# Performance work log

Hardware: AMD Instinct MI355X
Metric: run time of the kernel (lower is better)

## Reference

```python
import jax, jax.numpy as jnp
import numpy as np

EMB = 768
HEADS = 8
HEAD_DIM = EMB // HEADS  # 96


def setup_inputs() -> dict:
    key = jax.random.key(0)
    k1, k2, k3, k4, k5 = jax.random.split(key, 5)
    N, S = 2, 4096
    values = jax.random.normal(k1, (N, S, EMB), dtype=jnp.float32)
    keys = jax.random.normal(k2, (N, S, EMB), dtype=jnp.float32)
    query = jax.random.normal(k3, (N, S, EMB), dtype=jnp.float32)
    # fc_out: nn.Linear(emb_size, emb_size) -> weight [out,in], bias [out]
    bound = 1.0 / np.sqrt(EMB)
    fc_w = jax.random.uniform(k4, (EMB, EMB), dtype=jnp.float32, minval=-bound, maxval=bound)
    fc_b = jax.random.uniform(k5, (EMB,), dtype=jnp.float32, minval=-bound, maxval=bound)
    return {"values": values, "keys": keys, "query": query, "fc_w": fc_w, "fc_b": fc_b}


def reference(values, keys, query, fc_w, fc_b):
    # NOTE: original forward never uses the per-head q/k/v Linear layers;
    # it reshapes raw inputs into heads directly. We reproduce that faithfully.
    N, Sq, _ = query.shape
    # [N, S, E] -> [N, H, S, D]
    q = query.reshape(N, Sq, HEADS, HEAD_DIM).transpose(0, 2, 1, 3)
    k = keys.reshape(N, -1, HEADS, HEAD_DIM).transpose(0, 2, 1, 3)
    v = values.reshape(N, -1, HEADS, HEAD_DIM).transpose(0, 2, 1, 3)
    scale = 1.0 / np.sqrt(HEAD_DIM).astype(np.float32)
    scores = jnp.einsum('nhqd,nhkd->nhqk', q, k) * scale  # [N,H,Sq,Sk]
    p = jax.nn.softmax(scores, axis=-1)
    x = jnp.einsum('nhqk,nhkd->nhqd', p, v)  # [N,H,Sq,D]
    x = x.transpose(0, 2, 1, 3).reshape(N, Sq, EMB)
    return x @ fc_w.T + fc_b
```

## Files before the change

kernel.cpp:

```cpp
#include <hip/hip_runtime.h>
#include <hip/hip_bf16.h>

#define S_LEN 4096
#define EMB 768
#define NHEAD 8
#define HDIM 96

typedef short bf16x8 __attribute__((ext_vector_type(8)));
typedef float f32x4 __attribute__((ext_vector_type(4)));
typedef float f32x16 __attribute__((ext_vector_type(16)));

__device__ __forceinline__ short f2bf(float x) {
  union { float f; unsigned u; } v; v.f = x;
  unsigned r = v.u + 0x7fffu + ((v.u >> 16) & 1u);
  return (short)(r >> 16);
}

__device__ __forceinline__ short f2bfh(float x) {
  union { __hip_bfloat16 h; short s; } u;
  u.h = __float2bfloat16(x);
  return u.s;
}

#define GLOAD_LDS16(gp, lp)                                              \
  __builtin_amdgcn_global_load_lds(                                      \
      (const __attribute__((address_space(1))) unsigned int*)(gp),       \
      (__attribute__((address_space(3))) unsigned int*)(lp), 16, 0, 0)

__global__ __launch_bounds__(256) void prep_kernel(const float* __restrict__ K,
                                                   const float* __restrict__ W,
                                                   const float* __restrict__ V,
                                                   short* __restrict__ KVT,
                                                   short* __restrict__ Wb) {
  __shared__ short tlbuf[6656];
  int b = blockIdx.x;
  int tid = threadIdx.x;
  if (b < 288) {
    int t = b * 256 + tid;
    size_t off = (size_t)t * 8;
    float4 a = *(const float4*)(W + off);
    float4 bq = *(const float4*)(W + off + 4);
    bf16x8 r;
    r[0]=f2bf(a.x);  r[1]=f2bf(a.y);  r[2]=f2bf(a.z);  r[3]=f2bf(a.w);
    r[4]=f2bf(bq.x); r[5]=f2bf(bq.y); r[6]=f2bf(bq.z); r[7]=f2bf(bq.w);
    *(bf16x8*)(Wb + off) = r;
    return;
  }
  int bb = b - 288;
  int n = bb >> 9, h = (bb >> 6) & 7, st = bb & 63;
  int s0 = st * 64;
  short* KVp = KVT + ((size_t)((n * NHEAD + h) * 64 + st)) * 12288;

  const float* kp = K + ((size_t)(n * S_LEN + s0)) * EMB + h * HDIM;
  #pragma unroll
  for (int k = 0; k < 6; ++k) {
    int idx = k * 256 + tid;
    int fidx = idx * 4;
    int s = fidx / 96, d = fidx % 96;
    float4 a = *(const float4*)(kp + (size_t)s * EMB + d);
    short* t4 = &tlbuf[s * 104 + d];
    t4[0] = f2bf(a.x); t4[1] = f2bf(a.y); t4[2] = f2bf(a.z); t4[3] = f2bf(a.w);
  }
  __syncthreads();
  #pragma unroll
  for (int i = 0; i < 3; ++i) {
    int u = i * 256 + tid;
    int c = u >> 7, rem = u & 127, key = rem >> 1, h8 = rem & 1;
    int db = c * 16 + h8 * 8;
    short4 lo = *(const short4*)&tlbuf[key * 104 + db];
    short4 hi4 = *(const short4*)&tlbuf[key * 104 + db + 4];
    bf16x8 r;
    r[0]=lo.x; r[1]=lo.y; r[2]=lo.z; r[3]=lo.w;
    r[4]=hi4.x; r[5]=hi4.y; r[6]=hi4.z; r[7]=hi4.w;
    *(bf16x8*)(KVp + (size_t)u * 8) = r;
  }
  __syncthreads();

  const float* vp = V + ((size_t)(n * S_LEN + s0)) * EMB + h * HDIM;
  #pragma unroll
  for (int k = 0; k < 6; ++k) {
    int idx = k * 256 + tid;
    int fidx = idx * 4;
    int s = fidx / 96, d = fidx % 96;
    float4 a = *(const float4*)(vp + (size_t)s * EMB + d);
    tlbuf[(d + 0) * 68 + s] = f2bf(a.x);
    tlbuf[(d + 1) * 68 + s] = f2bf(a.y);
    tlbuf[(d + 2) * 68 + s] = f2bf(a.z);
    tlbuf[(d + 3) * 68 + s] = f2bf(a.w);
  }
  __syncthreads();
  #pragma unroll
  for (int i = 0; i < 3; ++i) {
    int u = i * 256 + tid;
    int slice = u / 192;
    int rem = u - slice * 192;
    int dt = rem >> 6, hi2 = (rem >> 5) & 1, d5 = rem & 31;
    int d = dt * 32 + d5;
    int kb = 16 * slice + 4 * hi2;
    short4 lo = *(const short4*)&tlbuf[d * 68 + kb];
    short4 hi4 = *(const short4*)&tlbuf[d * 68 + kb + 8];
    bf16x8 r;
    r[0]=lo.x; r[1]=lo.y; r[2]=lo.z; r[3]=lo.w;
    r[4]=hi4.x; r[5]=hi4.y; r[6]=hi4.z; r[7]=hi4.w;
    *(bf16x8*)(KVp + 6144 + (size_t)u * 8) = r;
  }
}

template<int NKG>
__global__ __launch_bounds__(256, 3) void attn_kernel(const float* __restrict__ Q,
                                                      const short* __restrict__ KVT,
                                                      short* __restrict__ Xb,
                                                      float* __restrict__ Op,
                                                      float* __restrict__ lp) {
  __shared__ __align__(16) char smem[49152];
  constexpr int ITERS = S_LEN / NKG / 64;
  int L = blockIdx.x;
  int bb = L & 511;
  int kg = L >> 9;
  int h = bb & 7, j = bb >> 3;
  int n = j >> 5, qt = j & 31;
  int q0 = qt * 128;
  int tid = threadIdx.x;
  int w = tid >> 6, lane = tid & 63, l31 = lane & 31, hi = lane >> 5;

  const float kAdj = 0.14724512f;
  bf16x8 qf[6];
  {
    const float* qp = Q + ((size_t)(n * S_LEN + q0 + w * 32 + l31)) * EMB + h * HDIM + 8 * hi;
    #pragma unroll
    for (int c = 0; c < 6; ++c) {
      float4 a = *(const float4*)(qp + 16 * c);
      float4 bq = *(const float4*)(qp + 16 * c + 4);
      bf16x8 r;
      r[0]=f2bf(a.x*kAdj);  r[1]=f2bf(a.y*kAdj);  r[2]=f2bf(a.z*kAdj);  r[3]=f2bf(a.w*kAdj);
      r[4]=f2bf(bq.x*kAdj); r[5]=f2bf(bq.y*kAdj); r[6]=f2bf(bq.z*kAdj); r[7]=f2bf(bq.w*kAdj);
      qf[c] = r;
    }
  }

  const short* gKV = KVT + ((size_t)((n * NHEAD + h) * 64 + kg * ITERS)) * 12288
                        + (size_t)(w * 6) * 512 + lane * 8;
  char* ldsw = smem + w * 6144;

  #pragma unroll
  for (int i = 0; i < 6; ++i)
    GLOAD_LDS16(gKV + i * 512, ldsw + i * 1024);
  __syncthreads();

  f32x16 o[3];
  #pragma unroll
  for (int dt = 0; dt < 3; ++dt) o[dt] = (f32x16){};
  float tsl = 0.f;

  int cur = 0;
  #pragma unroll 1
  for (int t = 0; t < ITERS; ++t) {
    if (t < ITERS - 1) {
      const short* src = gKV + (size_t)(t + 1) * 12288;
      char* dst = ldsw + (cur ^ 1) * 24576;
      #pragma unroll
      for (int i = 0; i < 6; ++i)
        GLOAD_LDS16(src + i * 512, dst + i * 1024);
    }
    const char* kbl = smem + cur * 24576;
    const char* vbl = kbl + 12288;

    f32x16 s0 = (f32x16){}, s1 = (f32x16){};
    __builtin_amdgcn_s_setprio(1);
    #pragma unroll
    for (int c = 0; c < 6; ++c) {
      bf16x8 kf = *(const bf16x8*)(kbl + c * 2048 + l31 * 32 + hi * 16);
      s0 = __builtin_amdgcn_mfma_f32_32x32x16_bf16(kf, qf[c], s0, 0, 0, 0);
    }
    #pragma unroll
    for (int c = 0; c < 6; ++c) {
      bf16x8 kf = *(const bf16x8*)(kbl + c * 2048 + 1024 + l31 * 32 + hi * 16);
      s1 = __builtin_amdgcn_mfma_f32_32x32x16_bf16(kf, qf[c], s1, 0, 0, 0);
    }
    __builtin_amdgcn_s_setprio(0);

    #pragma unroll
    for (int r = 0; r < 16; ++r) { s0[r] = __builtin_amdgcn_exp2f(s0[r]); tsl += s0[r]; }
    #pragma unroll
    for (int r = 0; r < 16; ++r) { s1[r] = __builtin_amdgcn_exp2f(s1[r]); tsl += s1[r]; }

    #pragma unroll
    for (int ksub = 0; ksub < 2; ++ksub) {
      const f32x16& s = ksub ? s1 : s0;
      #pragma unroll
      for (int ks = 0; ks < 2; ++ks) {
        unsigned d0, d1, d2, d3;
        asm("v_cvt_pk_bf16_f32 %0, %1, %2" : "=v"(d0) : "v"(s[8*ks+0]), "v"(s[8*ks+1]));
        asm("v_cvt_pk_bf16_f32 %0, %1, %2" : "=v"(d1) : "v"(s[8*ks+2]), "v"(s[8*ks+3]));
        asm("v_cvt_pk_bf16_f32 %0, %1, %2" : "=v"(d2) : "v"(s[8*ks+4]), "v"(s[8*ks+5]));
        asm("v_cvt_pk_bf16_f32 %0, %1, %2" : "=v"(d3) : "v"(s[8*ks+6]), "v"(s[8*ks+7]));
        union { unsigned u[4]; bf16x8 v; } pu;
        pu.u[0] = d0; pu.u[1] = d1; pu.u[2] = d2; pu.u[3] = d3;
        int slice = 2 * ksub + ks;
        __builtin_amdgcn_s_setprio(1);
        #pragma unroll
        for (int dt = 0; dt < 3; ++dt) {
          bf16x8 vf = *(const bf16x8*)(vbl + (slice * 3 + dt) * 1024 + hi * 512 + l31 * 16);
          o[dt] = __builtin_amdgcn_mfma_f32_32x32x16_bf16(pu.v, vf, o[dt], 0, 0, 0);
        }
        __builtin_amdgcn_s_setprio(0);
      }
    }
    __syncthreads();
    cur ^= 1;
  }

  float lcol = tsl + __shfl_xor(tsl, 32, 64);

  if constexpr (NKG > 1) {
    float* op = Op + (size_t)L * 12288;
    #pragma unroll
    for (int p = 0; p < 4; ++p) {
      #pragma unroll
      for (int jj = 0; jj < 4; ++jj) {
        int qrow = w * 32 + 8 * p + 4 * hi + jj;
        op[(size_t)qrow * 96 + l31]      = o[0][4*p+jj];
        op[(size_t)qrow * 96 + 32 + l31] = o[1][4*p+jj];
        op[(size_t)qrow * 96 + 64 + l31] = o[2][4*p+jj];
      }
    }
    if (hi == 0) lp[(size_t)L * 128 + w * 32 + l31] = lcol;
  } else {
    __syncthreads();
    float* bcf = (float*)smem;
    if (hi == 0) bcf[w * 32 + l31] = 1.0f / lcol;
    __syncthreads();
    #pragma unroll
    for (int p = 0; p < 4; ++p) {
      #pragma unroll
      for (int jj = 0; jj < 4; ++jj) {
        int qr = 8 * p + 4 * hi + jj;
        float iv = bcf[w * 32 + qr];
        short* xp = Xb + ((size_t)(n * S_LEN + q0 + w * 32 + qr)) * EMB + h * HDIM + l31;
        xp[0]  = f2bfh(o[0][4*p+jj] * iv);
        xp[32] = f2bfh(o[1][4*p+jj] * iv);
        xp[64] = f2bfh(o[2][4*p+jj] * iv);
      }
    }
  }
}

__global__ __launch_bounds__(256) void combine_kernel(const float* __restrict__ Op,
                                                      const float* __restrict__ lp,
                                                      short* __restrict__ Xb,
                                                      int nkg) {
  int b = blockIdx.x;
  int h = b & 7, j = b >> 3, n = j >> 5, qt = j & 31;
  int q0 = qt * 128;
  int tid = threadIdx.x;
  #pragma unroll 1
  for (int i = 0; i < 12; ++i) {
    int idx = (i * 256 + tid) * 4;
    int qr = idx / 96, d = idx - qr * 96;
    float ax = 0.f, ay = 0.f, az = 0.f, aw = 0.f, l = 0.f;
    for (int kg = 0; kg < nkg; ++kg) {
      size_t blk = (size_t)(kg * 512 + b);
      float4 v = *(const float4*)(Op + blk * 12288 + idx);
      ax += v.x; ay += v.y; az += v.z; aw += v.w;
      l += lp[blk * 128 + qr];
    }
    float iv = 1.0f / l;
    short4 r;
    r.x = f2bfh(ax * iv); r.y = f2bfh(ay * iv);
    r.z = f2bfh(az * iv); r.w = f2bfh(aw * iv);
    *(short4*)(Xb + ((size_t)(n * S_LEN + q0 + qr)) * EMB + h * HDIM + d) = r;
  }
}

__global__ __launch_bounds__(256) void fc_kernel(const short* __restrict__ Xb,
                                                 const short* __restrict__ Wb,
                                                 const float* __restrict__ bias,
                                                 float* __restrict__ out) {
  int m0 = blockIdx.x * 64, j0 = blockIdx.y * 64;
  int tid = threadIdx.x;
  int w = tid >> 6, lane = tid & 63, lr = lane & 15, lg = lane >> 4;
  f32x4 acc[4];
  #pragma unroll
  for (int jt = 0; jt < 4; ++jt) acc[jt] = (f32x4){0.f, 0.f, 0.f, 0.f};
  const short* xp = Xb + (size_t)(m0 + w * 16 + lr) * EMB + 8 * lg;
  const short* wp = Wb + (size_t)(j0 + lr) * EMB + 8 * lg;
  #pragma unroll 1
  for (int kt = 0; kt < 24; ++kt) {
    bf16x8 a = *(const bf16x8*)(xp + kt * 32);
    #pragma unroll
    for (int jt = 0; jt < 4; ++jt) {
      bf16x8 bw = *(const bf16x8*)(wp + (size_t)(jt * 16) * EMB + kt * 32);
      acc[jt] = __builtin_amdgcn_mfma_f32_16x16x32_bf16(a, bw, acc[jt], 0, 0, 0);
    }
  }
  #pragma unroll
  for (int jt = 0; jt < 4; ++jt) {
    float bb = bias[j0 + jt * 16 + lr];
    #pragma unroll
    for (int i = 0; i < 4; ++i)
      out[(size_t)(m0 + w * 16 + 4 * lg + i) * EMB + j0 + jt * 16 + lr] = acc[jt][i] + bb;
  }
}

extern "C" void kernel_launch(void* const* d_in, const int* in_sizes, int n_in,
                              void* d_out, int out_size, void* d_ws, size_t ws_size,
                              hipStream_t stream) {
  (void)in_sizes; (void)n_in; (void)out_size;
  const float* V = (const float*)d_in[0];
  const float* K = (const float*)d_in[1];
  const float* Q = (const float*)d_in[2];
  const float* W = (const float*)d_in[3];
  const float* B = (const float*)d_in[4];
  float* out = (float*)d_out;
  short* KVT = (short*)d_ws;
  short* Wb  = KVT + 12582912;
  short* Xb  = Wb + 589824;
  size_t base_bytes = (size_t)(12582912 + 589824 + 6291456) * 2;
  size_t part_bytes = (size_t)2 * 512 * (12288 + 128) * 4;
  prep_kernel<<<1312, 256, 0, stream>>>(K, W, V, KVT, Wb);
  if (ws_size >= base_bytes + part_bytes) {
    float* Op = (float*)((char*)d_ws + base_bytes);
    float* lp = Op + (size_t)2 * 512 * 12288;
    attn_kernel<2><<<1024, 256, 0, stream>>>(Q, KVT, Xb, Op, lp);
    combine_kernel<<<512, 256, 0, stream>>>(Op, lp, Xb, 2);
  } else {
    attn_kernel<1><<<512, 256, 0, stream>>>(Q, KVT, Xb, nullptr, nullptr);
  }
  fc_kernel<<<dim3(128, 12), 256, 0, stream>>>(Xb, Wb, B, out);
}
```

Baseline: 217.0 us.

## Split K/V prep into separate blocks and relayout K for contiguous lane reads

The prep kernel now gives K and V tiles their own blocks, 2336 instead of 1312, so each block handles one tensor and needs fewer barriers, with more parallelism. K is stored in an order where each lane's 16-byte fragment sits at lane*16, which makes the attention kernel's K reads from LDS simple and contiguous. The exp-sum accumulation becomes a tree reduction, shortening the serial add chain. The risks are a layout mismatch between producer and consumer, and the extra overhead of launching more blocks.

Result: no change. 216.7 us (-0.2%).

```diff
diff --git a/kernel.cpp b/kernel.cpp
--- a/kernel.cpp
+++ b/kernel.cpp
@@ -46,36 +46,41 @@
     *(bf16x8*)(Wb + off) = r;
     return;
   }
-  int bb = b - 288;
+  if (b < 1312) {
+    int bb = b - 288;
+    int n = bb >> 9, h = (bb >> 6) & 7, st = bb & 63;
+    int s0 = st * 64;
+    const float* kp = K + ((size_t)(n * S_LEN + s0)) * EMB + h * HDIM;
+    #pragma unroll
+    for (int k = 0; k < 6; ++k) {
+      int idx = k * 256 + tid;
+      int fidx = idx * 4;
+      int s = fidx / 96, d = fidx % 96;
+      float4 a = *(const float4*)(kp + (size_t)s * EMB + d);
+      short* t4 = &tlbuf[s * 104 + d];
+      t4[0] = f2bf(a.x); t4[1] = f2bf(a.y); t4[2] = f2bf(a.z); t4[3] = f2bf(a.w);
+    }
+    __syncthreads();
+    short* KVp = KVT + ((size_t)((n * NHEAD + h) * 64 + st)) * 12288;
+    #pragma unroll
+    for (int i = 0; i < 3; ++i) {
+      int u = i * 256 + tid;
+      int c = u >> 7, rem = u & 127;
+      int ksub = (rem >> 6) & 1, hi2 = (rem >> 5) & 1, l31 = rem & 31;
+      int key = ksub * 32 + l31;
+      int db = c * 16 + hi2 * 8;
+      short4 lo = *(const short4*)&tlbuf[key * 104 + db];
+      short4 hi4 = *(const short4*)&tlbuf[key * 104 + db + 4];
+      bf16x8 r;
+      r[0]=lo.x; r[1]=lo.y; r[2]=lo.z; r[3]=lo.w;
+      r[4]=hi4.x; r[5]=hi4.y; r[6]=hi4.z; r[7]=hi4.w;
+      *(bf16x8*)(KVp + (size_t)u * 8) = r;
+    }
+    return;
+  }
+  int bb = b - 1312;
   int n = bb >> 9, h = (bb >> 6) & 7, st = bb & 63;
   int s0 = st * 64;
-  short* KVp = KVT + ((size_t)((n * NHEAD + h) * 64 + st)) * 12288;
-
-  const float* kp = K + ((size_t)(n * S_LEN + s0)) * EMB + h * HDIM;
-  #pragma unroll
-  for (int k = 0; k < 6; ++k) {
-    int idx = k * 256 + tid;
-    int fidx = idx * 4;
-    int s = fidx / 96, d = fidx % 96;
-    float4 a = *(const float4*)(kp + (size_t)s * EMB + d);
-    short* t4 = &tlbuf[s * 104 + d];
-    t4[0] = f2bf(a.x); t4[1] = f2bf(a.y); t4[2] = f2bf(a.z); t4[3] = f2bf(a.w);
-  }
-  __syncthreads();
-  #pragma unroll
-  for (int i = 0; i < 3; ++i) {
-    int u = i * 256 + tid;
-    int c = u >> 7, rem = u & 127, key = rem >> 1, h8 = rem & 1;
-    int db = c * 16 + h8 * 8;
-    short4 lo = *(const short4*)&tlbuf[key * 104 + db];
-    short4 hi4 = *(const short4*)&tlbuf[key * 104 + db + 4];
-    bf16x8 r;
-    r[0]=lo.x; r[1]=lo.y; r[2]=lo.z; r[3]=lo.w;
-    r[4]=hi4.x; r[5]=hi4.y; r[6]=hi4.z; r[7]=hi4.w;
-    *(bf16x8*)(KVp + (size_t)u * 8) = r;
-  }
-  __syncthreads();
-
   const float* vp = V + ((size_t)(n * S_LEN + s0)) * EMB + h * HDIM;
   #pragma unroll
   for (int k = 0; k < 6; ++k) {
@@ -89,6 +94,7 @@
     tlbuf[(d + 3) * 68 + s] = f2bf(a.w);
   }
   __syncthreads();
+  short* KVp = KVT + ((size_t)((n * NHEAD + h) * 64 + st)) * 12288 + 6144;
   #pragma unroll
   for (int i = 0; i < 3; ++i) {
     int u = i * 256 + tid;
@@ -102,7 +108,7 @@
     bf16x8 r;
     r[0]=lo.x; r[1]=lo.y; r[2]=lo.z; r[3]=lo.w;
     r[4]=hi4.x; r[5]=hi4.y; r[6]=hi4.z; r[7]=hi4.w;
-    *(bf16x8*)(KVp + 6144 + (size_t)u * 8) = r;
+    *(bf16x8*)(KVp + (size_t)u * 8) = r;
   }
 }
 
@@ -169,20 +175,27 @@
     __builtin_amdgcn_s_setprio(1);
     #pragma unroll
     for (int c = 0; c < 6; ++c) {
-      bf16x8 kf = *(const bf16x8*)(kbl + c * 2048 + l31 * 32 + hi * 16);
+      bf16x8 kf = *(const bf16x8*)(kbl + c * 2048 + lane * 16);
       s0 = __builtin_amdgcn_mfma_f32_32x32x16_bf16(kf, qf[c], s0, 0, 0, 0);
     }
     #pragma unroll
     for (int c = 0; c < 6; ++c) {
-      bf16x8 kf = *(const bf16x8*)(kbl + c * 2048 + 1024 + l31 * 32 + hi * 16);
+      bf16x8 kf = *(const bf16x8*)(kbl + c * 2048 + 1024 + lane * 16);
       s1 = __builtin_amdgcn_mfma_f32_32x32x16_bf16(kf, qf[c], s1, 0, 0, 0);
     }
     __builtin_amdgcn_s_setprio(0);
 
     #pragma unroll
-    for (int r = 0; r < 16; ++r) { s0[r] = __builtin_amdgcn_exp2f(s0[r]); tsl += s0[r]; }
-    #pragma unroll
-    for (int r = 0; r < 16; ++r) { s1[r] = __builtin_amdgcn_exp2f(s1[r]); tsl += s1[r]; }
+    for (int r = 0; r < 16; ++r) s0[r] = __builtin_amdgcn_exp2f(s0[r]);
+    #pragma unroll
+    for (int r = 0; r < 16; ++r) s1[r] = __builtin_amdgcn_exp2f(s1[r]);
+    {
+      float a0 = (s0[0]+s0[1]) + (s0[2]+s0[3]), a1 = (s0[4]+s0[5]) + (s0[6]+s0[7]);
+      float a2 = (s0[8]+s0[9]) + (s0[10]+s0[11]), a3 = (s0[12]+s0[13]) + (s0[14]+s0[15]);
+      float b0 = (s1[0]+s1[1]) + (s1[2]+s1[3]), b1 = (s1[4]+s1[5]) + (s1[6]+s1[7]);
+      float b2 = (s1[8]+s1[9]) + (s1[10]+s1[11]), b3 = (s1[12]+s1[13]) + (s1[14]+s1[15]);
+      tsl += ((a0+a1) + (a2+a3)) + ((b0+b1) + (b2+b3));
+    }
 
     #pragma unroll
     for (int ksub = 0; ksub < 2; ++ksub) {
@@ -317,7 +330,7 @@
   short* Xb  = Wb + 589824;
   size_t base_bytes = (size_t)(12582912 + 589824 + 6291456) * 2;
   size_t part_bytes = (size_t)2 * 512 * (12288 + 128) * 4;
-  prep_kernel<<<1312, 256, 0, stream>>>(K, W, V, KVT, Wb);
+  prep_kernel<<<2336, 256, 0, stream>>>(K, W, V, KVT, Wb);
   if (ws_size >= base_bytes + part_bytes) {
     float* Op = (float*)((char*)d_ws + base_bytes);
     float* lp = Op + (size_t)2 * 512 * 12288;
```
